# Kernel tuning notes

Measured on AMD Instinct MI355X. Metric: run time of the kernel, lower is better.

## Reference

```python
import jax, jax.numpy as jnp
import numpy as np

B, D, H, W, C = 2, 8, 128, 128, 64
HEADS, DH = 4, 16
EPS = 1e-12  # torch F.normalize eps


def setup_inputs() -> dict:
    key = jax.random.key(0)
    ks = jax.random.split(key, 8)
    rn = lambda k, shp, s: jax.random.normal(k, shp, jnp.float32) * s
    return {
        "x_in": rn(ks[0], (B, D, H, W, C), 1.0),
        "Wq": rn(ks[1], (C, HEADS * DH), 0.05),
        "Wk": rn(ks[2], (C, HEADS * DH), 0.05),
        "Wv": rn(ks[3], (C, HEADS * DH), 0.05),
        "rescale": jnp.ones((HEADS, 1, 1), jnp.float32),
        "Wproj": rn(ks[4], (HEADS * DH, C), 0.05),
        "bproj": jnp.zeros((C,), jnp.float32),
        "Wpos1": rn(ks[5], (C, 1, 3, 3, 3), 0.1),
        "Wpos2": rn(ks[6], (C, 1, 3, 3, 3), 0.1),
    }


def _l2norm(x):
    # torch F.normalize(p=2, dim=-1): x / max(||x||, eps)
    return x / jnp.maximum(jnp.linalg.norm(x, axis=-1, keepdims=True), EPS)


def _dwconv3d(x, w):
    # depthwise Conv3d, kernel 3, stride 1, padding 1, groups = channels
    return jax.lax.conv_general_dilated(
        x, w, (1, 1, 1), 'SAME',
        dimension_numbers=('NCDHW', 'OIDHW', 'NCDHW'),
        feature_group_count=w.shape[0])


def reference(x_in, Wq, Wk, Wv, rescale, Wproj, bproj, Wpos1, Wpos2):
    b, d, h, w, c = x_in.shape
    n = d * h * w
    x = x_in.reshape(b, n, c)
    v_inp = x @ Wv                                   # [b, n, heads*dh]
    # [b, heads, dh, n] layout (attention over channel dim)
    q = jnp.transpose((x @ Wq).reshape(b, n, HEADS, DH), (0, 2, 3, 1))
    k = jnp.transpose((x @ Wk).reshape(b, n, HEADS, DH), (0, 2, 3, 1))
    v = jnp.transpose(v_inp.reshape(b, n, HEADS, DH), (0, 2, 3, 1))
    q = _l2norm(q)
    k = _l2norm(k)
    attn = jnp.einsum('bhdn,bhen->bhde', k, q) * rescale  # [b, heads, dh, dh]
    attn = jax.nn.softmax(attn, axis=-1)
    out = jnp.einsum('bhde,bhen->bhdn', attn, v)          # [b, heads, dh, n]
    out = jnp.transpose(out, (0, 3, 1, 2)).reshape(b, n, HEADS * DH)
    out_c = (out @ Wproj + bproj).reshape(b, d, h, w, c)
    # positional branch: depthwise conv -> GELU -> depthwise conv on v_inp
    vv = jnp.transpose(v_inp.reshape(b, d, h, w, c), (0, 4, 1, 2, 3))  # NCDHW
    p = _dwconv3d(vv, Wpos1)
    p = jax.nn.gelu(p, approximate=False)
    p = _dwconv3d(p, Wpos2)
    out_p = jnp.transpose(p, (0, 2, 3, 4, 1))
    return out_c + out_p
```

## Files before the change

kernel.cpp:

```cpp
#include <hip/hip_runtime.h>
#include <math.h>

#define DD 8
#define HH 128
#define WW2 128
#define NPT 131072
#define NTOT 262144
#define NBK 8

typedef __attribute__((ext_vector_type(8))) short short8;
typedef __attribute__((ext_vector_type(4))) float f32x4;
typedef __attribute__((ext_vector_type(4))) unsigned short u16x4;
typedef __attribute__((ext_vector_type(8))) unsigned short u16x8;
typedef unsigned short u16;

static const size_t OFF_P1  = 0;
static const size_t OFF_P2  = 33554432;
static const size_t OFF_V   = 67108864;
static const size_t OFF_PW  = 100663296;
static const size_t OFF_PM  = 100687872;
static const size_t OFF_FLAG= 100704256;
static const size_t OFF_CW  = 100704768;
static const size_t OFF_PART= 134217728;
#define SP_F    0
#define WQ_F    65536
#define WK_F    69632
#define WV_F    73728
#define CW_WPROJ 0
#define CW_WPOS1 4096
#define CW_WPOS2 5824
#define CW_RESC  7552
#define CW_BPROJ 7556
#define CW_ATT   7680

__device__ __forceinline__ float bf2f(u16 u){
  unsigned int x = ((unsigned int)u) << 16;
  return __builtin_bit_cast(float, x);
}
__device__ __forceinline__ u16 f2bf(float f){
  unsigned int x = __builtin_bit_cast(unsigned int, f);
  unsigned int r = (x + 0x7fffu + ((x >> 16) & 1u)) >> 16;
  return (u16)r;
}

__device__ __forceinline__ float fgelu(float o){
  float z  = o * 0.70710678118654752f;
  float az = fabsf(z);
  float t1 = __builtin_amdgcn_rcpf(fmaf(0.3275911f, az, 1.f));
  float poly = t1 * fmaf(t1, fmaf(t1, fmaf(t1, fmaf(t1, 1.061405429f,
               -1.453152027f), 1.421413741f), -0.284496736f), 0.254829592f);
  float ex = __expf(-z * z);
  float er = 1.f - poly * ex;
  er = (z < 0.f) ? -er : er;
  return 0.5f * o * (1.f + er);
}

__device__ __forceinline__ int probe_isf32(const void* x, int t){
  u16 u = ((const u16*)x)[2 * (t & 63)];
  int e = (u >> 7) & 0xFF;
  int plaus = (u == 0) || (u == 0x8000u) || (e >= 100 && e <= 130);
  unsigned long long m = __ballot(plaus);
  return (__popcll(m) < 48) ? 1 : 0;
}

__global__ __launch_bounds__(256) void k_prep(const void* __restrict__ x,
    const void* __restrict__ Wproj, const void* __restrict__ rescale,
    const void* __restrict__ bproj, const void* __restrict__ Wpos1,
    const void* __restrict__ Wpos2, const void* __restrict__ Wq,
    const void* __restrict__ Wk, const void* __restrict__ Wv,
    int* __restrict__ flag, float* __restrict__ cw, float* __restrict__ gpart,
    u16* __restrict__ packW){
  __shared__ int sflag;
  int t = threadIdx.x, blk = blockIdx.x;
  if (t < 64){
    int f = probe_isf32(x, t);
    if (t == 0) sflag = f;
  }
  __syncthreads();
  int isf32 = sflag;
  if (blk < 32){
    for (int i = blk * 2048 + t; i < (blk + 1) * 2048; i += 256)
      gpart[i] = 0.f;
    if (blk == 0){
      if (t == 0) *flag = isf32;
      auto conv = [&](const void* src, float* dst, int n){
        for (int i = t; i < n; i += 256)
          dst[i] = isf32 ? ((const float*)src)[i] : bf2f(((const u16*)src)[i]);
      };
      conv(Wproj, cw + CW_WPROJ, 4096);
      conv(Wpos1, cw + CW_WPOS1, 1728);
      conv(Wpos2, cw + CW_WPOS2, 1728);
      conv(rescale, cw + CW_RESC, 4);
      conv(bproj,   cw + CW_BPROJ, 64);
      conv(Wq, gpart + WQ_F, 4096);
      conv(Wk, gpart + WK_F, 4096);
      conv(Wv, gpart + WV_F, 4096);
    }
  } else {
    int o = (blk - 32) * 256 + t;
    int f = o >> 9, l = (o >> 3) & 63, j = o & 7;
    int tt = f >> 1, s = f & 1;
    int k = s * 32 + (l >> 4) * 8 + j;
    int n = tt * 16 + (l & 15);
    int idx = k * 64 + n;
    float val = isf32 ? ((const float*)Wv)[idx] : bf2f(((const u16*)Wv)[idx]);
    packW[o] = f2bf(val);
  }
}

__device__ __forceinline__ short8 ld8_adapt(const void* p, size_t idx, int isf32){
  if (!isf32) return *(const short8*)((const u16*)p + idx);
  const float4* f = (const float4*)((const float*)p + idx);
  float4 u = f[0], v2 = f[1];
  short8 r;
  r[0] = (short)f2bf(u.x);  r[1] = (short)f2bf(u.y);
  r[2] = (short)f2bf(u.z);  r[3] = (short)f2bf(u.w);
  r[4] = (short)f2bf(v2.x); r[5] = (short)f2bf(v2.y);
  r[6] = (short)f2bf(v2.z); r[7] = (short)f2bf(v2.w);
  return r;
}

__global__ __launch_bounds__(512) void k_qkv(const void* __restrict__ x,
                                             const int* __restrict__ flag,
                                             const u16* __restrict__ packW,
                                             u16* __restrict__ vT,
                                             float* __restrict__ Sp){
  __shared__ u16 sXT[64][136];
  int isf32 = *flag;
  int wave = threadIdx.x >> 6, lane = threadIdx.x & 63;
  int m = lane & 15, quad = lane >> 4;
  const short8* bw = (const short8*)packW;
  short8 bv[8];
#pragma unroll
  for (int f = 0; f < 8; f++) bv[f] = bw[f * 64 + lane];
  int c1 = wave >> 1, c2p = (wave & 1) * 2;
  f32x4 aS[2];
  aS[0] = (f32x4)(0.f); aS[1] = (f32x4)(0.f);

  int pbase = blockIdx.x * 512;
  int b = pbase >> 17;

  for (int s = 0; s < 4; s++){
    int p0 = pbase + s * 128 + wave * 16;
    size_t rowbase = (size_t)(p0 + m) * 64;
    short8 a0 = ld8_adapt(x, rowbase + quad * 8, isf32);
    short8 a1 = ld8_adapt(x, rowbase + 32 + quad * 8, isf32);
    f32x4 av[4];
#pragma unroll
    for (int t = 0; t < 4; t++) av[t] = (f32x4)(0.f);
#pragma unroll
    for (int t = 0; t < 4; t++){
      av[t] = __builtin_amdgcn_mfma_f32_16x16x32_bf16(a0, bv[t * 2 + 0], av[t], 0, 0, 0);
      av[t] = __builtin_amdgcn_mfma_f32_16x16x32_bf16(a1, bv[t * 2 + 1], av[t], 0, 0, 0);
    }
    int nloc = p0 & (NPT - 1);
#pragma unroll
    for (int t = 0; t < 4; t++){
      u16x4 pk;
#pragma unroll
      for (int r = 0; r < 4; r++) pk[r] = f2bf(av[t][r]);
      *(u16x4*)(vT + ((size_t)(b * 64 + t * 16 + m)) * NPT + nloc + quad * 4) = pk;
    }
    if (s) __syncthreads();
#pragma unroll
    for (int j = 0; j < 8; j++){
      sXT[quad * 8 + j][wave * 16 + m]      = (u16)a0[j];
      sXT[32 + quad * 8 + j][wave * 16 + m] = (u16)a1[j];
    }
    __syncthreads();
#pragma unroll
    for (int ks = 0; ks < 4; ks++){
      short8 fA  = *(const short8*)&sXT[c1 * 16 + m][ks * 32 + quad * 8];
      short8 fB0 = *(const short8*)&sXT[(c2p + 0) * 16 + m][ks * 32 + quad * 8];
      short8 fB1 = *(const short8*)&sXT[(c2p + 1) * 16 + m][ks * 32 + quad * 8];
      aS[0] = __builtin_amdgcn_mfma_f32_16x16x32_bf16(fA, fB0, aS[0], 0, 0, 0);
      aS[1] = __builtin_amdgcn_mfma_f32_16x16x32_bf16(fA, fB1, aS[1], 0, 0, 0);
    }
  }
  int bk = blockIdx.x & (NBK - 1);
  float* Sb = Sp + (size_t)(bk * 2 + b) * 4096;
#pragma unroll
  for (int tt = 0; tt < 2; tt++)
#pragma unroll
    for (int r = 0; r < 4; r++)
      atomicAdd(&Sb[(c1 * 16 + quad * 4 + r) * 64 + (c2p + tt) * 16 + m], aS[tt][r]);
}

__device__ void attn_side(int blk, int t, float* smem,
                          const float* __restrict__ Sp, const float* __restrict__ wqk,
                          const float* __restrict__ cw, float* __restrict__ Aout){
  float* sS  = smem;
  float* sWh = smem + 4160;
  float* sT  = smem + 5184;
  float* sG  = smem + 6208;
  float* sNq = smem + 6464;
  float* sNk = smem + 6480;
  int b = blk >> 2, h = blk & 3;
  for (int i = t; i < 4096; i += 256){
    float s = 0.f;
#pragma unroll
    for (int bk = 0; bk < NBK; bk++) s += Sp[(size_t)(bk * 2 + b) * 4096 + i];
    sS[(i >> 6) * 65 + (i & 63)] = s;
  }
  for (int i = t; i < 1024; i += 256)
    sWh[i] = wqk[(i >> 4) * 64 + h * 16 + (i & 15)];
  __syncthreads();
  int cc = t & 63, eg = t >> 6;
  {
    float a0 = 0.f, a1 = 0.f, a2 = 0.f, a3 = 0.f;
    for (int c2 = 0; c2 < 64; c2++){
      float sv = sS[cc * 65 + c2];
      a0 = fmaf(sv, sWh[c2 * 16 + eg * 4 + 0], a0);
      a1 = fmaf(sv, sWh[c2 * 16 + eg * 4 + 1], a1);
      a2 = fmaf(sv, sWh[c2 * 16 + eg * 4 + 2], a2);
      a3 = fmaf(sv, sWh[c2 * 16 + eg * 4 + 3], a3);
    }
    sT[cc * 16 + eg * 4 + 0] = a0;
    sT[cc * 16 + eg * 4 + 1] = a1;
    sT[cc * 16 + eg * 4 + 2] = a2;
    sT[cc * 16 + eg * 4 + 3] = a3;
  }
  __syncthreads();
  if (t < 16){
    float a = 0.f;
    for (int c = 0; c < 64; c++) a += sWh[c * 16 + t] * sT[c * 16 + t];
    sNq[t] = a;
  }
  __syncthreads();
  for (int i = t; i < 1024; i += 256)
    sWh[i] = wqk[4096 + (i >> 4) * 64 + h * 16 + (i & 15)];
  __syncthreads();
  {
    int d = t >> 4, e = t & 15;
    float a = 0.f;
    for (int c = 0; c < 64; c++) a += sWh[c * 16 + d] * sT[c * 16 + e];
    sG[d * 16 + e] = a;
  }
  __syncthreads();
  {
    float a0 = 0.f, a1 = 0.f, a2 = 0.f, a3 = 0.f;
    for (int c2 = 0; c2 < 64; c2++){
      float sv = sS[cc * 65 + c2];
      a0 = fmaf(sv, sWh[c2 * 16 + eg * 4 + 0], a0);
      a1 = fmaf(sv, sWh[c2 * 16 + eg * 4 + 1], a1);
      a2 = fmaf(sv, sWh[c2 * 16 + eg * 4 + 2], a2);
      a3 = fmaf(sv, sWh[c2 * 16 + eg * 4 + 3], a3);
    }
    __syncthreads();
    sT[cc * 16 + eg * 4 + 0] = a0;
    sT[cc * 16 + eg * 4 + 1] = a1;
    sT[cc * 16 + eg * 4 + 2] = a2;
    sT[cc * 16 + eg * 4 + 3] = a3;
  }
  __syncthreads();
  if (t < 16){
    float a = 0.f;
    for (int c = 0; c < 64; c++) a += sWh[c * 16 + t] * sT[c * 16 + t];
    sNk[t] = a;
  }
  __syncthreads();
  if (t < 16){
    int d = t;
    float nk = fmaxf(sqrtf(sNk[d]), 1e-12f);
    float rs = cw[CW_RESC + h];
    float lg[16]; float mx = -1e30f;
#pragma unroll
    for (int e = 0; e < 16; e++){
      float nq = fmaxf(sqrtf(sNq[e]), 1e-12f);
      float L = sG[d * 16 + e] / (nk * nq) * rs;
      lg[e] = L; mx = fmaxf(mx, L);
    }
    float sum = 0.f;
#pragma unroll
    for (int e = 0; e < 16; e++){ lg[e] = expf(lg[e] - mx); sum += lg[e]; }
    float inv = 1.f / sum;
#pragma unroll
    for (int e = 0; e < 16; e++)
      Aout[((b * 4 + h) << 8) + d * 16 + e] = lg[e] * inv;
  }
}

__device__ void fold_side(int b, int t, float* sM,
                          const float* __restrict__ Aout, const float* __restrict__ Wprojf,
                          const float* __restrict__ Wvf, u16* __restrict__ packM){
  for (int i = t; i < 4096; i += 256){
    int he = i >> 6, c = i & 63;
    int h = he >> 4, e = he & 15;
    float acc = 0.f;
#pragma unroll
    for (int d = 0; d < 16; d++)
      acc += Aout[b * 1024 + h * 256 + d * 16 + e] * Wprojf[(h * 16 + d) * 64 + c];
    sM[i] = acc;
  }
  __syncthreads();
  for (int i = t; i < 4096; i += 256){
    int f = i >> 9, l = (i >> 3) & 63, j = i & 7;
    int t4 = f >> 1, s2 = f & 1;
    int k = s2 * 32 + (l >> 4) * 8 + j;
    int n = t4 * 16 + (l & 15);
    float acc = 0.f;
#pragma unroll 8
    for (int he = 0; he < 64; he++)
      acc += Wvf[k * 64 + he] * sM[he * 64 + n];
    packM[b * 4096 + i] = f2bf(acc);
  }
}

template <bool GELU>
__global__ __launch_bounds__(256, 4) void k_dwconv(const u16* __restrict__ src,
    const float* __restrict__ wpos, u16* __restrict__ dst,
    const float* __restrict__ Sp, const float* __restrict__ wqk,
    const float* __restrict__ cw, float* __restrict__ Aout,
    const float* __restrict__ Wprojf, const float* __restrict__ Wvf,
    u16* __restrict__ packM){
  constexpr int SMSZ = GELU ? 6496 : 4096;
  __shared__ float smem[SMSZ];
  if (blockIdx.x == 64){
    int side = blockIdx.z * 16 + blockIdx.y;
    if (GELU){
      if (side < 8) attn_side(side, threadIdx.x, smem, Sp, wqk, cw, Aout);
    } else {
      if (side < 2) fold_side(side, threadIdx.x, smem, Aout, Wprojf, Wvf, packM);
    }
    return;
  }
  int xi = threadIdx.x & 15, ty = threadIdx.x >> 4;
  int zp = ty >> 2, yq = ty & 3;
  int x0 = xi * 8;
  int c  = blockIdx.x;
  int y0 = blockIdx.y * 8 + yq * 2;
  int b  = blockIdx.z;
  int z0 = zp * 2;
  const float* wg = wpos + c * 27;
  float w27[27];
#pragma unroll
  for (int i = 0; i < 27; i++) w27[i] = wg[i];
  const u16* plane = src + (size_t)(b * 64 + c) * NPT;
  float acc[2][2][8];
#pragma unroll
  for (int dz = 0; dz < 2; dz++)
#pragma unroll
    for (int dy = 0; dy < 2; dy++)
#pragma unroll
      for (int xx = 0; xx < 8; xx++) acc[dz][dy][xx] = 0.f;
#pragma unroll
  for (int izz = 0; izz < 4; izz++){
    int zz = z0 - 1 + izz;
    if (zz < 0 || zz >= DD) continue;
    const u16* pz = plane + zz * 16384;
#pragma unroll
    for (int iyy = 0; iyy < 4; iyy++){
      int yyr = y0 - 1 + iyy;
      int yc = yyr < 0 ? 0 : (yyr > HH - 1 ? HH - 1 : yyr);
      float vmask = (yyr == yc) ? 1.f : 0.f;
      const u16* rp = pz + yc * 128 + x0;
      short8 mid = *(const short8*)rp;
      u16 lft = 0, rgt = 0;
      if (x0 > 0)   lft = rp[-1];
      if (x0 < 120) rgt = rp[8];
      float row[10];
      row[0] = bf2f(lft) * vmask;
#pragma unroll
      for (int e = 0; e < 8; e++) row[1 + e] = bf2f((u16)mid[e]) * vmask;
      row[9] = bf2f(rgt) * vmask;
#pragma unroll
      for (int dzi = 0; dzi < 2; dzi++){
        int kd = izz - dzi;
        if (kd < 0 || kd > 2) continue;
#pragma unroll
        for (int dyi = 0; dyi < 2; dyi++){
          int kh = iyy - dyi;
          if (kh < 0 || kh > 2) continue;
#pragma unroll
          for (int kw = 0; kw < 3; kw++){
            float w = w27[kd * 9 + kh * 3 + kw];
#pragma unroll
            for (int xx = 0; xx < 8; xx++)
              acc[dzi][dyi][xx] = fmaf(row[xx + kw], w, acc[dzi][dyi][xx]);
          }
        }
      }
    }
  }
#pragma unroll
  for (int dzi = 0; dzi < 2; dzi++){
    int zo = z0 + dzi;
#pragma unroll
    for (int dyi = 0; dyi < 2; dyi++){
      int yo = y0 + dyi;
      u16x8 pk;
#pragma unroll
      for (int xx = 0; xx < 8; xx++){
        float o = acc[dzi][dyi][xx];
        if (GELU) o = fgelu(o);
        pk[xx] = f2bf(o);
      }
      *(u16x8*)(dst + (size_t)(b * 64 + c) * NPT + zo * 16384 + yo * 128 + x0) = pk;
    }
  }
}

__global__ __launch_bounds__(256) void k_final(const void* __restrict__ x,
                                               const int* __restrict__ flag,
                                               const u16* __restrict__ packM,
                                               const float* __restrict__ bprojf,
                                               const u16* __restrict__ p2T,
                                               float* __restrict__ out){
  int isf32 = *flag;
  int wave = threadIdx.x >> 6, lane = threadIdx.x & 63;
  int m = lane & 15, quad = lane >> 4;
  int p0 = blockIdx.x * 64 + wave * 16;
  int b = p0 >> 17;
  int nloc = p0 & (NPT - 1);
  size_t rowbase = (size_t)(p0 + m) * 64;
  short8 a0 = ld8_adapt(x, rowbase + quad * 8, isf32);
  short8 a1 = ld8_adapt(x, rowbase + 32 + quad * 8, isf32);
  const short8* bm = (const short8*)(packM + (size_t)b * 4096);
  f32x4 acc[4];
#pragma unroll
  for (int t = 0; t < 4; t++) acc[t] = (f32x4)(0.f);
#pragma unroll
  for (int t = 0; t < 4; t++){
    short8 b0 = bm[(t * 2 + 0) * 64 + lane];
    short8 b1 = bm[(t * 2 + 1) * 64 + lane];
    acc[t] = __builtin_amdgcn_mfma_f32_16x16x32_bf16(a0, b0, acc[t], 0, 0, 0);
    acc[t] = __builtin_amdgcn_mfma_f32_16x16x32_bf16(a1, b1, acc[t], 0, 0, 0);
  }
#pragma unroll
  for (int t = 0; t < 4; t++){
    int c = t * 16 + m;
    float bias = bprojf[c];
    u16x4 pv = *(const u16x4*)(p2T + (size_t)(b * 64 + c) * NPT + nloc + quad * 4);
#pragma unroll
    for (int r = 0; r < 4; r++){
      size_t p = (size_t)p0 + quad * 4 + r;
      out[p * 64 + c] = acc[t][r] + bias + bf2f(pv[r]);
    }
  }
}

extern "C" void kernel_launch(void* const* d_in, const int* in_sizes, int n_in,
                              void* d_out, int out_size, void* d_ws, size_t ws_size,
                              hipStream_t stream){
  (void)in_sizes; (void)n_in; (void)out_size; (void)ws_size;
  const void* x      = d_in[0];
  const void* Wq     = d_in[1];
  const void* Wk     = d_in[2];
  const void* Wv     = d_in[3];
  const void* rescale= d_in[4];
  const void* Wproj  = d_in[5];
  const void* bproj  = d_in[6];
  const void* Wpos1  = d_in[7];
  const void* Wpos2  = d_in[8];

  char* ws = (char*)d_ws;
  u16* p1T   = (u16*)(ws + OFF_P1);
  u16* p2T   = (u16*)(ws + OFF_P2);
  u16* vT    = (u16*)(ws + OFF_V);
  u16* packW = (u16*)(ws + OFF_PW);
  u16* packM = (u16*)(ws + OFF_PM);
  int* flag  = (int*)(ws + OFF_FLAG);
  float* cw  = (float*)(ws + OFF_CW);
  float* part= (float*)(ws + OFF_PART);
  float* Sp  = part + SP_F;
  float* wqk = part + WQ_F;
  float* Wvf = part + WV_F;
  float* Aout= cw + CW_ATT;
  float* out = (float*)d_out;

  k_prep<<<48, 256, 0, stream>>>(x, Wproj, rescale, bproj, Wpos1, Wpos2, Wq, Wk, Wv,
                                 flag, cw, Sp, packW);
  k_qkv<<<NTOT / 512, 512, 0, stream>>>(x, flag, packW, vT, Sp);
  k_dwconv<true><<<dim3(65, 16, 2), 256, 0, stream>>>(vT, cw + CW_WPOS1, p1T,
      Sp, wqk, cw, Aout, cw + CW_WPROJ, Wvf, packM);
  k_dwconv<false><<<dim3(65, 16, 2), 256, 0, stream>>>(p1T, cw + CW_WPOS2, p2T,
      Sp, wqk, cw, Aout, cw + CW_WPROJ, Wvf, packM);
  k_final<<<NTOT / 64, 256, 0, stream>>>(x, flag, packM, cw + CW_BPROJ, p2T, out);
}
```

Measured before the change: 275.7 us.

## Prefetch qkv inputs, split attention side work into kernels, shuffle dwconv halos

In k_qkv, the next tile's x rows are loaded before the current tile's S-accumulation, so global latency overlaps the MFMA work. The attention softmax and projection-fold side work move out of the dwconv kernels into two small standalone kernels. This removes the extra block column and the larger shared-memory footprint from the convolution launches, but adds two serial tiny launches. The dwconv kernel now issues all 16 row loads up front and gets left/right halo values through lane shuffles instead of scalar loads, with launch bounds lowered to 3 blocks per CU.

Result: slower. 298.5 us (+8.3%).

```diff
diff --git a/kernel.cpp b/kernel.cpp
--- a/kernel.cpp
+++ b/kernel.cpp
@@ -120,6 +120,15 @@
   return r;
 }
 
+__device__ __forceinline__ short8 pack8(float4 u, float4 v2){
+  short8 r;
+  r[0] = (short)f2bf(u.x);  r[1] = (short)f2bf(u.y);
+  r[2] = (short)f2bf(u.z);  r[3] = (short)f2bf(u.w);
+  r[4] = (short)f2bf(v2.x); r[5] = (short)f2bf(v2.y);
+  r[6] = (short)f2bf(v2.z); r[7] = (short)f2bf(v2.w);
+  return r;
+}
+
 __global__ __launch_bounds__(512) void k_qkv(const void* __restrict__ x,
                                              const int* __restrict__ flag,
                                              const u16* __restrict__ packW,
@@ -140,11 +149,12 @@
   int pbase = blockIdx.x * 512;
   int b = pbase >> 17;
 
+  size_t rb0 = (size_t)(pbase + wave * 16 + m) * 64;
+  short8 a0 = ld8_adapt(x, rb0 + quad * 8, isf32);
+  short8 a1 = ld8_adapt(x, rb0 + 32 + quad * 8, isf32);
+
   for (int s = 0; s < 4; s++){
     int p0 = pbase + s * 128 + wave * 16;
-    size_t rowbase = (size_t)(p0 + m) * 64;
-    short8 a0 = ld8_adapt(x, rowbase + quad * 8, isf32);
-    short8 a1 = ld8_adapt(x, rowbase + 32 + quad * 8, isf32);
     f32x4 av[4];
 #pragma unroll
     for (int t = 0; t < 4; t++) av[t] = (f32x4)(0.f);
@@ -160,6 +170,19 @@
 #pragma unroll
       for (int r = 0; r < 4; r++) pk[r] = f2bf(av[t][r]);
       *(u16x4*)(vT + ((size_t)(b * 64 + t * 16 + m)) * NPT + nloc + quad * 4) = pk;
+    }
+    float4 pf0a, pf0b, pf1a, pf1b; short8 ps0, ps1;
+    if (s < 3){
+      size_t rbn = (size_t)(pbase + (s + 1) * 128 + wave * 16 + m) * 64;
+      if (isf32){
+        const float4* f0 = (const float4*)((const float*)x + rbn + quad * 8);
+        pf0a = f0[0]; pf0b = f0[1];
+        const float4* f1 = (const float4*)((const float*)x + rbn + 32 + quad * 8);
+        pf1a = f1[0]; pf1b = f1[1];
+      } else {
+        ps0 = *(const short8*)((const u16*)x + rbn + quad * 8);
+        ps1 = *(const short8*)((const u16*)x + rbn + 32 + quad * 8);
+      }
     }
     if (s) __syncthreads();
 #pragma unroll
@@ -176,6 +199,10 @@
       aS[0] = __builtin_amdgcn_mfma_f32_16x16x32_bf16(fA, fB0, aS[0], 0, 0, 0);
       aS[1] = __builtin_amdgcn_mfma_f32_16x16x32_bf16(fA, fB1, aS[1], 0, 0, 0);
     }
+    if (s < 3){
+      if (isf32){ a0 = pack8(pf0a, pf0b); a1 = pack8(pf1a, pf1b); }
+      else      { a0 = ps0;               a1 = ps1; }
+    }
   }
   int bk = blockIdx.x & (NBK - 1);
   float* Sb = Sp + (size_t)(bk * 2 + b) * 4096;
@@ -186,15 +213,15 @@
       atomicAdd(&Sb[(c1 * 16 + quad * 4 + r) * 64 + (c2p + tt) * 16 + m], aS[tt][r]);
 }
 
-__device__ void attn_side(int blk, int t, float* smem,
-                          const float* __restrict__ Sp, const float* __restrict__ wqk,
-                          const float* __restrict__ cw, float* __restrict__ Aout){
-  float* sS  = smem;
-  float* sWh = smem + 4160;
-  float* sT  = smem + 5184;
-  float* sG  = smem + 6208;
-  float* sNq = smem + 6464;
-  float* sNk = smem + 6480;
+__global__ __launch_bounds__(256) void k_attn_h(const float* __restrict__ Sp,
+    const float* __restrict__ wqk, const float* __restrict__ cw,
+    float* __restrict__ Aout){
+  __shared__ float sS[64 * 65];
+  __shared__ float sWh[1024];
+  __shared__ float sT[1024];
+  __shared__ float sG[256];
+  __shared__ float sNq[16], sNk[16];
+  int blk = blockIdx.x, t = threadIdx.x;
   int b = blk >> 2, h = blk & 3;
   for (int i = t; i < 4096; i += 256){
     float s = 0.f;
@@ -280,16 +307,18 @@
   }
 }
 
-__device__ void fold_side(int b, int t, float* sM,
-                          const float* __restrict__ Aout, const float* __restrict__ Wprojf,
-                          const float* __restrict__ Wvf, u16* __restrict__ packM){
+__global__ __launch_bounds__(256) void k_fold(const float* __restrict__ Aout,
+    const float* __restrict__ cw, const float* __restrict__ Wvf,
+    u16* __restrict__ packM){
+  __shared__ float sM[4096];
+  int b = blockIdx.x, t = threadIdx.x;
   for (int i = t; i < 4096; i += 256){
     int he = i >> 6, c = i & 63;
     int h = he >> 4, e = he & 15;
     float acc = 0.f;
 #pragma unroll
     for (int d = 0; d < 16; d++)
-      acc += Aout[b * 1024 + h * 256 + d * 16 + e] * Wprojf[(h * 16 + d) * 64 + c];
+      acc += Aout[b * 1024 + h * 256 + d * 16 + e] * cw[CW_WPROJ + (h * 16 + d) * 64 + c];
     sM[i] = acc;
   }
   __syncthreads();
@@ -307,23 +336,8 @@
 }
 
 template <bool GELU>
-__global__ __launch_bounds__(256, 4) void k_dwconv(const u16* __restrict__ src,
-    const float* __restrict__ wpos, u16* __restrict__ dst,
-    const float* __restrict__ Sp, const float* __restrict__ wqk,
-    const float* __restrict__ cw, float* __restrict__ Aout,
-    const float* __restrict__ Wprojf, const float* __restrict__ Wvf,
-    u16* __restrict__ packM){
-  constexpr int SMSZ = GELU ? 6496 : 4096;
-  __shared__ float smem[SMSZ];
-  if (blockIdx.x == 64){
-    int side = blockIdx.z * 16 + blockIdx.y;
-    if (GELU){
-      if (side < 8) attn_side(side, threadIdx.x, smem, Sp, wqk, cw, Aout);
-    } else {
-      if (side < 2) fold_side(side, threadIdx.x, smem, Aout, Wprojf, Wvf, packM);
-    }
-    return;
-  }
+__global__ __launch_bounds__(256, 3) void k_dwconv(const u16* __restrict__ src,
+    const float* __restrict__ wpos, u16* __restrict__ dst){
   int xi = threadIdx.x & 15, ty = threadIdx.x >> 4;
   int zp = ty >> 2, yq = ty & 3;
   int x0 = xi * 8;
@@ -336,6 +350,23 @@
 #pragma unroll
   for (int i = 0; i < 27; i++) w27[i] = wg[i];
   const u16* plane = src + (size_t)(b * 64 + c) * NPT;
+
+  short8 raw[16];
+  float  msk[16];
+#pragma unroll
+  for (int iz = 0; iz < 4; iz++){
+    int zz = z0 - 1 + iz;
+    int zc = zz < 0 ? 0 : (zz > DD - 1 ? DD - 1 : zz);
+    float zm = (zz == zc) ? 1.f : 0.f;
+#pragma unroll
+    for (int iy = 0; iy < 4; iy++){
+      int yy = y0 - 1 + iy;
+      int yc = yy < 0 ? 0 : (yy > HH - 1 ? HH - 1 : yy);
+      raw[iz * 4 + iy] = *(const short8*)(plane + zc * 16384 + yc * 128 + x0);
+      msk[iz * 4 + iy] = zm * ((yy == yc) ? 1.f : 0.f);
+    }
+  }
+
   float acc[2][2][8];
 #pragma unroll
   for (int dz = 0; dz < 2; dz++)
@@ -343,33 +374,29 @@
     for (int dy = 0; dy < 2; dy++)
 #pragma unroll
       for (int xx = 0; xx < 8; xx++) acc[dz][dy][xx] = 0.f;
-#pragma unroll
-  for (int izz = 0; izz < 4; izz++){
-    int zz = z0 - 1 + izz;
-    if (zz < 0 || zz >= DD) continue;
-    const u16* pz = plane + zz * 16384;
-#pragma unroll
-    for (int iyy = 0; iyy < 4; iyy++){
-      int yyr = y0 - 1 + iyy;
-      int yc = yyr < 0 ? 0 : (yyr > HH - 1 ? HH - 1 : yyr);
-      float vmask = (yyr == yc) ? 1.f : 0.f;
-      const u16* rp = pz + yc * 128 + x0;
-      short8 mid = *(const short8*)rp;
-      u16 lft = 0, rgt = 0;
-      if (x0 > 0)   lft = rp[-1];
-      if (x0 < 120) rgt = rp[8];
+
+#pragma unroll
+  for (int iz = 0; iz < 4; iz++){
+#pragma unroll
+    for (int iy = 0; iy < 4; iy++){
+      short8 mid = raw[iz * 4 + iy];
+      float m = msk[iz * 4 + iy];
       float row[10];
-      row[0] = bf2f(lft) * vmask;
-#pragma unroll
-      for (int e = 0; e < 8; e++) row[1 + e] = bf2f((u16)mid[e]) * vmask;
-      row[9] = bf2f(rgt) * vmask;
+#pragma unroll
+      for (int e = 0; e < 8; e++) row[1 + e] = bf2f((u16)mid[e]);
+      float lf = __shfl_up(row[8], 1);
+      float rg = __shfl_down(row[1], 1);
+      row[0] = (xi > 0)  ? lf : 0.f;
+      row[9] = (xi < 15) ? rg : 0.f;
+#pragma unroll
+      for (int e = 0; e < 10; e++) row[e] *= m;
 #pragma unroll
       for (int dzi = 0; dzi < 2; dzi++){
-        int kd = izz - dzi;
+        int kd = iz - dzi;
         if (kd < 0 || kd > 2) continue;
 #pragma unroll
         for (int dyi = 0; dyi < 2; dyi++){
-          int kh = iyy - dyi;
+          int kh = iy - dyi;
           if (kh < 0 || kh > 2) continue;
 #pragma unroll
           for (int kw = 0; kw < 3; kw++){
@@ -471,9 +498,9 @@
   k_prep<<<48, 256, 0, stream>>>(x, Wproj, rescale, bproj, Wpos1, Wpos2, Wq, Wk, Wv,
                                  flag, cw, Sp, packW);
   k_qkv<<<NTOT / 512, 512, 0, stream>>>(x, flag, packW, vT, Sp);
-  k_dwconv<true><<<dim3(65, 16, 2), 256, 0, stream>>>(vT, cw + CW_WPOS1, p1T,
-      Sp, wqk, cw, Aout, cw + CW_WPROJ, Wvf, packM);
-  k_dwconv<false><<<dim3(65, 16, 2), 256, 0, stream>>>(p1T, cw + CW_WPOS2, p2T,
-      Sp, wqk, cw, Aout, cw + CW_WPROJ, Wvf, packM);
+  k_attn_h<<<8, 256, 0, stream>>>(Sp, wqk, cw, Aout);
+  k_fold<<<2, 256, 0, stream>>>(Aout, cw, Wvf, packM);
+  k_dwconv<true><<<dim3(64, 16, 2), 256, 0, stream>>>(vT, cw + CW_WPOS1, p1T);
+  k_dwconv<false><<<dim3(64, 16, 2), 256, 0, stream>>>(p1T, cw + CW_WPOS2, p2T);
   k_final<<<NTOT / 64, 256, 0, stream>>>(x, flag, packM, cw + CW_BPROJ, p2T, out);
 }
```
